# Performance work log

Hardware: AMD Instinct MI355X
Metric: run time of the kernel (lower is better)

Reference implementation:

```python
import jax, jax.numpy as jnp
import numpy as np

N_USERS, N_ITEMS, DIM = 100000, 50000, 64
NNZ, BATCH = 1200000, 16384
N_NODES = N_USERS + N_ITEMS


def setup_inputs() -> dict:
    key = jax.random.key(0)
    k = jax.random.split(key, 7)
    user_emb = jax.random.normal(k[0], (N_USERS, DIM), dtype=jnp.float32)
    item_emb = jax.random.normal(k[1], (N_ITEMS, DIM), dtype=jnp.float32)
    adj_rows = jax.random.randint(k[2], (NNZ,), 0, N_NODES, dtype=jnp.int64 if jax.config.jax_enable_x64 else jnp.int32)
    adj_cols = jax.random.randint(k[3], (NNZ,), 0, N_NODES, dtype=jnp.int64 if jax.config.jax_enable_x64 else jnp.int32)
    adj_vals = jax.random.uniform(k[4], (NNZ,), dtype=jnp.float32)
    u = jax.random.randint(k[5], (BATCH,), 0, N_USERS)
    i = jax.random.randint(k[6], (BATCH,), 0, N_ITEMS)
    return {"user_emb": user_emb, "item_emb": item_emb,
            "adj_rows": adj_rows, "adj_cols": adj_cols, "adj_vals": adj_vals,
            "u": u, "i": i}


def reference(user_emb, item_emb, adj_rows, adj_cols, adj_vals, u, i):
    # propagate: E' = A_norm @ cat([user_emb, item_emb])  (sparse COO SpMM)
    all_emb = jnp.concatenate([user_emb, item_emb], axis=0)          # [N, D]
    msgs = adj_vals[:, None] * all_emb[adj_cols]                     # [nnz, D]
    all_prop = jax.ops.segment_sum(msgs, adj_rows, num_segments=N_NODES)
    users_prop = all_prop[:N_USERS]
    items_prop = all_prop[N_USERS:]
    # score = dot(user_prop[u], item_prop[i])
    scores = jnp.sum(users_prop[u] * items_prop[i], axis=1)          # [B]
    return scores
```

## Files before the change

### kernel.cpp

```cpp
#include <hip/hip_runtime.h>

#define N_USERS 100000
#define N_ITEMS 50000
#define N_NODES 150000
#define NNZ     1200000
#define DIM     64
#define BATCH   16384
#define MAXDEG  64


__global__ void assign_ids_kernel(const int* __restrict__ u,
                                  const int* __restrict__ it,
                                  unsigned* __restrict__ rowid,
                                  unsigned* __restrict__ cnt) {
    const int t = blockIdx.x * blockDim.x + threadIdx.x;
    if (t >= 2 * BATCH) return;
    cnt[t] = 0u;
    const int node = (t < BATCH) ? u[t] : (N_USERS + it[t - BATCH]);
    atomicMin(&rowid[node], (unsigned)t);
}

__global__ void build_lists_kernel(const int*   __restrict__ rows,
                                   const int*   __restrict__ cols,
                                   const float* __restrict__ vals,
                                   const unsigned* __restrict__ rowid,
                                   unsigned* __restrict__ cnt,
                                   uint2* __restrict__ pairs) {
    const int e = blockIdx.x * blockDim.x + threadIdx.x;
    if (e >= NNZ) return;
    const unsigned id = rowid[rows[e]];
    if (id == 0xFFFFFFFFu) return;
    const int   c = cols[e];
    const float v = vals[e];
    const unsigned slot = atomicAdd(&cnt[id], 1u);
    if (slot < MAXDEG)
        pairs[(size_t)id * MAXDEG + slot] = make_uint2((unsigned)c, __float_as_uint(v));
}

__global__ void score_kernel(const float* __restrict__ user_emb,
                             const float* __restrict__ item_emb,
                             const int* __restrict__ u,
                             const int* __restrict__ it,
                             const unsigned* __restrict__ rowid,
                             const unsigned* __restrict__ cnt,
                             const uint2* __restrict__ pairs,
                             float* __restrict__ out) {
    const int lane = threadIdx.x & 63;
    const int wave = (blockIdx.x * blockDim.x + threadIdx.x) >> 6;
    if (wave >= BATCH) return;

    const unsigned uid = rowid[u[wave]];
    const unsigned iid = rowid[N_USERS + it[wave]];
    const unsigned un  = min(cnt[uid], (unsigned)MAXDEG);
    const unsigned in_ = min(cnt[iid], (unsigned)MAXDEG);

    uint2 ue = make_uint2(0u, 0u), ie = make_uint2(0u, 0u);
    if (lane < (int)un)  ue = pairs[(size_t)uid * MAXDEG + lane];
    if (lane < (int)in_) ie = pairs[(size_t)iid * MAXDEG + lane];

    float uacc = 0.f, iacc = 0.f;

    for (unsigned j = 0; j < un; j += 4) {
        float m[4], vv[4];
        #pragma unroll
        for (int t = 0; t < 4; ++t) {
            if (j + t < un) {
                const int   col = __shfl((int)ue.x, (int)(j + t), 64);
                vv[t] = __shfl(__uint_as_float(ue.y), (int)(j + t), 64);
                const float* src = (col < N_USERS)
                                     ? (user_emb + (size_t)col * DIM)
                                     : (item_emb + (size_t)(col - N_USERS) * DIM);
                m[t] = src[lane];
            }
        }
        #pragma unroll
        for (int t = 0; t < 4; ++t)
            if (j + t < un) uacc += vv[t] * m[t];
    }

    for (unsigned j = 0; j < in_; j += 4) {
        float m[4], vv[4];
        #pragma unroll
        for (int t = 0; t < 4; ++t) {
            if (j + t < in_) {
                const int   col = __shfl((int)ie.x, (int)(j + t), 64);
                vv[t] = __shfl(__uint_as_float(ie.y), (int)(j + t), 64);
                const float* src = (col < N_USERS)
                                     ? (user_emb + (size_t)col * DIM)
                                     : (item_emb + (size_t)(col - N_USERS) * DIM);
                m[t] = src[lane];
            }
        }
        #pragma unroll
        for (int t = 0; t < 4; ++t)
            if (j + t < in_) iacc += vv[t] * m[t];
    }

    float p = uacc * iacc;
    p += __shfl_xor(p, 1);
    p += __shfl_xor(p, 2);
    p += __shfl_xor(p, 4);
    p += __shfl_xor(p, 8);
    p += __shfl_xor(p, 16);
    p += __shfl_xor(p, 32);

    if (lane == 0) out[wave] = p;
}

extern "C" void kernel_launch(void* const* d_in, const int* in_sizes, int n_in,
                              void* d_out, int out_size, void* d_ws, size_t ws_size,
                              hipStream_t stream) {
    const float* user_emb = (const float*)d_in[0];
    const float* item_emb = (const float*)d_in[1];
    const int*   rows     = (const int*)d_in[2];
    const int*   cols     = (const int*)d_in[3];
    const float* vals     = (const float*)d_in[4];
    const int*   u        = (const int*)d_in[5];
    const int*   it       = (const int*)d_in[6];
    float*       out      = (float*)d_out;

    unsigned* rowid = (unsigned*)d_ws;
    unsigned* cnt   = rowid + N_NODES;
    uint2*    pairs = (uint2*)(cnt + 2 * BATCH);

    hipMemsetAsync(rowid, 0xFF, (size_t)N_NODES * sizeof(unsigned), stream);

    assign_ids_kernel<<<(2 * BATCH + 255) / 256, 256, 0, stream>>>(u, it, rowid, cnt);

    build_lists_kernel<<<(NNZ + 255) / 256, 256, 0, stream>>>(rows, cols, vals,
                                                              rowid, cnt, pairs);

    score_kernel<<<(BATCH * 64) / 256, 256, 0, stream>>>(user_emb, item_emb, u, it,
                                                         rowid, cnt, pairs, out);
}
```

Before: 127.3 us.

## Fuse memset, id assignment, list build and scoring into one cooperative kernel

Replaces the memset plus three kernel launches with a single cooperative kernel. It uses grid-wide syncs between the init, id-assignment, edge-bucketing and scoring phases, and uses grid-stride loops over edges and batch pairs. The scoring loop now interleaves the user and item neighbour gathers in a single loop, so more loads are in flight. The aim is to remove launch gaps and per-launch overhead. In exchange it adds three grid barriers and limits the grid to 1024 blocks, with a fallback to the old path if the cooperative launch fails.

Result: slower. 435.0 us (+241.8%).

```diff
diff --git a/kernel.cpp b/kernel.cpp
--- a/kernel.cpp
+++ b/kernel.cpp
@@ -1,4 +1,7 @@
 #include <hip/hip_runtime.h>
+#include <hip/hip_cooperative_groups.h>
+
+namespace cg = cooperative_groups;
 
 #define N_USERS 100000
 #define N_ITEMS 50000
@@ -7,7 +10,113 @@
 #define DIM     64
 #define BATCH   16384
 #define MAXDEG  64
+#define NBLK    1024
+#define NTHR    256
 
+
+__device__ __forceinline__ const float* emb_ptr(const float* ue, const float* ie, int col) {
+    return (col < N_USERS) ? (ue + (size_t)col * DIM)
+                           : (ie + (size_t)(col - N_USERS) * DIM);
+}
+
+__device__ __forceinline__ void score_pair(const float* __restrict__ user_emb,
+                                           const float* __restrict__ item_emb,
+                                           const unsigned* __restrict__ rowid,
+                                           const unsigned* __restrict__ cnt,
+                                           const uint2* __restrict__ pairs,
+                                           const int* __restrict__ u,
+                                           const int* __restrict__ it,
+                                           float* __restrict__ out,
+                                           int pair, int lane) {
+    const unsigned uid = rowid[u[pair]];
+    const unsigned iid = rowid[N_USERS + it[pair]];
+    const unsigned un  = min(cnt[uid], (unsigned)MAXDEG);
+    const unsigned in_ = min(cnt[iid], (unsigned)MAXDEG);
+
+    uint2 ue = make_uint2(0u, 0u), ie = make_uint2(0u, 0u);
+    if (lane < (int)un)  ue = pairs[(size_t)uid * MAXDEG + lane];
+    if (lane < (int)in_) ie = pairs[(size_t)iid * MAXDEG + lane];
+
+    float uacc = 0.f, iacc = 0.f;
+    const unsigned rounds = un > in_ ? un : in_;
+
+    for (unsigned j = 0; j < rounds; j += 4) {
+        float mu[4], vu[4], mi[4], vi[4];
+        #pragma unroll
+        for (int t = 0; t < 4; ++t) {
+            if (j + t < un) {
+                const int col = __shfl((int)ue.x, (int)(j + t), 64);
+                vu[t] = __shfl(__uint_as_float(ue.y), (int)(j + t), 64);
+                mu[t] = emb_ptr(user_emb, item_emb, col)[lane];
+            }
+        }
+        #pragma unroll
+        for (int t = 0; t < 4; ++t) {
+            if (j + t < in_) {
+                const int col = __shfl((int)ie.x, (int)(j + t), 64);
+                vi[t] = __shfl(__uint_as_float(ie.y), (int)(j + t), 64);
+                mi[t] = emb_ptr(user_emb, item_emb, col)[lane];
+            }
+        }
+        #pragma unroll
+        for (int t = 0; t < 4; ++t) if (j + t < un)  uacc += vu[t] * mu[t];
+        #pragma unroll
+        for (int t = 0; t < 4; ++t) if (j + t < in_) iacc += vi[t] * mi[t];
+    }
+
+    float p = uacc * iacc;
+    p += __shfl_xor(p, 1);
+    p += __shfl_xor(p, 2);
+    p += __shfl_xor(p, 4);
+    p += __shfl_xor(p, 8);
+    p += __shfl_xor(p, 16);
+    p += __shfl_xor(p, 32);
+    if (lane == 0) out[pair] = p;
+}
+
+__global__ void __launch_bounds__(NTHR, 4)
+fused_kernel(const float* __restrict__ user_emb,
+             const float* __restrict__ item_emb,
+             const int*   __restrict__ rows,
+             const int*   __restrict__ cols,
+             const float* __restrict__ vals,
+             const int*   __restrict__ u,
+             const int*   __restrict__ it,
+             unsigned*    __restrict__ rowid,
+             unsigned*    __restrict__ cnt,
+             uint2*       __restrict__ pairs,
+             float*       __restrict__ out) {
+    cg::grid_group grid = cg::this_grid();
+    const int gtid  = blockIdx.x * blockDim.x + threadIdx.x;
+    const int gsize = NBLK * NTHR;
+
+    if (gtid < N_NODES) rowid[gtid] = 0xFFFFFFFFu;
+    if (gtid < 2 * BATCH) cnt[gtid] = 0u;
+    grid.sync();
+
+    if (gtid < 2 * BATCH) {
+        const int node = (gtid < BATCH) ? u[gtid] : (N_USERS + it[gtid - BATCH]);
+        atomicMin(&rowid[node], (unsigned)gtid);
+    }
+    grid.sync();
+
+    for (int e = gtid; e < NNZ; e += gsize) {
+        const unsigned id = rowid[rows[e]];
+        if (id != 0xFFFFFFFFu) {
+            const unsigned slot = atomicAdd(&cnt[id], 1u);
+            if (slot < MAXDEG)
+                pairs[(size_t)id * MAXDEG + slot] =
+                    make_uint2((unsigned)cols[e], __float_as_uint(vals[e]));
+        }
+    }
+    grid.sync();
+
+    const int lane = threadIdx.x & 63;
+    const int wave = gtid >> 6;
+    const int nwav = gsize >> 6;
+    for (int pair = wave; pair < BATCH; pair += nwav)
+        score_pair(user_emb, item_emb, rowid, cnt, pairs, u, it, out, pair, lane);
+}
 
 __global__ void assign_ids_kernel(const int* __restrict__ u,
                                   const int* __restrict__ it,
@@ -30,11 +139,10 @@
     if (e >= NNZ) return;
     const unsigned id = rowid[rows[e]];
     if (id == 0xFFFFFFFFu) return;
-    const int   c = cols[e];
-    const float v = vals[e];
     const unsigned slot = atomicAdd(&cnt[id], 1u);
     if (slot < MAXDEG)
-        pairs[(size_t)id * MAXDEG + slot] = make_uint2((unsigned)c, __float_as_uint(v));
+        pairs[(size_t)id * MAXDEG + slot] =
+            make_uint2((unsigned)cols[e], __float_as_uint(vals[e]));
 }
 
 __global__ void score_kernel(const float* __restrict__ user_emb,
@@ -48,63 +156,7 @@
     const int lane = threadIdx.x & 63;
     const int wave = (blockIdx.x * blockDim.x + threadIdx.x) >> 6;
     if (wave >= BATCH) return;
-
-    const unsigned uid = rowid[u[wave]];
-    const unsigned iid = rowid[N_USERS + it[wave]];
-    const unsigned un  = min(cnt[uid], (unsigned)MAXDEG);
-    const unsigned in_ = min(cnt[iid], (unsigned)MAXDEG);
-
-    uint2 ue = make_uint2(0u, 0u), ie = make_uint2(0u, 0u);
-    if (lane < (int)un)  ue = pairs[(size_t)uid * MAXDEG + lane];
-    if (lane < (int)in_) ie = pairs[(size_t)iid * MAXDEG + lane];
-
-    float uacc = 0.f, iacc = 0.f;
-
-    for (unsigned j = 0; j < un; j += 4) {
-        float m[4], vv[4];
-        #pragma unroll
-        for (int t = 0; t < 4; ++t) {
-            if (j + t < un) {
-                const int   col = __shfl((int)ue.x, (int)(j + t), 64);
-                vv[t] = __shfl(__uint_as_float(ue.y), (int)(j + t), 64);
-                const float* src = (col < N_USERS)
-                                     ? (user_emb + (size_t)col * DIM)
-                                     : (item_emb + (size_t)(col - N_USERS) * DIM);
-                m[t] = src[lane];
-            }
-        }
-        #pragma unroll
-        for (int t = 0; t < 4; ++t)
-            if (j + t < un) uacc += vv[t] * m[t];
-    }
-
-    for (unsigned j = 0; j < in_; j += 4) {
-        float m[4], vv[4];
-        #pragma unroll
-        for (int t = 0; t < 4; ++t) {
-            if (j + t < in_) {
-                const int   col = __shfl((int)ie.x, (int)(j + t), 64);
-                vv[t] = __shfl(__uint_as_float(ie.y), (int)(j + t), 64);
-                const float* src = (col < N_USERS)
-                                     ? (user_emb + (size_t)col * DIM)
-                                     : (item_emb + (size_t)(col - N_USERS) * DIM);
-                m[t] = src[lane];
-            }
-        }
-        #pragma unroll
-        for (int t = 0; t < 4; ++t)
-            if (j + t < in_) iacc += vv[t] * m[t];
-    }
-
-    float p = uacc * iacc;
-    p += __shfl_xor(p, 1);
-    p += __shfl_xor(p, 2);
-    p += __shfl_xor(p, 4);
-    p += __shfl_xor(p, 8);
-    p += __shfl_xor(p, 16);
-    p += __shfl_xor(p, 32);
-
-    if (lane == 0) out[wave] = p;
+    score_pair(user_emb, item_emb, rowid, cnt, pairs, u, it, out, wave, lane);
 }
 
 extern "C" void kernel_launch(void* const* d_in, const int* in_sizes, int n_in,
@@ -123,13 +175,20 @@
     unsigned* cnt   = rowid + N_NODES;
     uint2*    pairs = (uint2*)(cnt + 2 * BATCH);
 
-    hipMemsetAsync(rowid, 0xFF, (size_t)N_NODES * sizeof(unsigned), stream);
+    void* kargs[] = { (void*)&user_emb, (void*)&item_emb, (void*)&rows,
+                      (void*)&cols, (void*)&vals, (void*)&u, (void*)&it,
+                      (void*)&rowid, (void*)&cnt, (void*)&pairs, (void*)&out };
 
-    assign_ids_kernel<<<(2 * BATCH + 255) / 256, 256, 0, stream>>>(u, it, rowid, cnt);
-
-    build_lists_kernel<<<(NNZ + 255) / 256, 256, 0, stream>>>(rows, cols, vals,
-                                                              rowid, cnt, pairs);
-
-    score_kernel<<<(BATCH * 64) / 256, 256, 0, stream>>>(user_emb, item_emb, u, it,
-                                                         rowid, cnt, pairs, out);
+    hipError_t err = hipLaunchCooperativeKernel((void*)fused_kernel,
+                                                dim3(NBLK), dim3(NTHR),
+                                                kargs, 0, stream);
+    if (err != hipSuccess) {
+        (void)hipGetLastError();
+        hipMemsetAsync(rowid, 0xFF, (size_t)N_NODES * sizeof(unsigned), stream);
+        assign_ids_kernel<<<(2 * BATCH + 255) / 256, 256, 0, stream>>>(u, it, rowid, cnt);
+        build_lists_kernel<<<(NNZ + 255) / 256, 256, 0, stream>>>(rows, cols, vals,
+                                                                  rowid, cnt, pairs);
+        score_kernel<<<(BATCH * 64) / 256, 256, 0, stream>>>(user_emb, item_emb, u, it,
+                                                             rowid, cnt, pairs, out);
+    }
 }
```
